# Kernel optimization log

Measured on AMD Instinct MI355X. Metric: run time of the kernel, lower is better.

Reference implementation:

```python
import jax, jax.numpy as jnp
import numpy as np

ALPHA = 0.2  # tf.nn.leaky_relu default alpha
B, LATENT, T, N = 8, 256, 128, 768
F, L, E = 4, 3, 12288


def _causal_conv1d(x, w, b):
    # x: [B,T,Cin], w: [K,Cin,Cout] -> causal pad left by K-1
    k = w.shape[0]
    y = jax.lax.conv_general_dilated(x, w, (1,), ((k - 1, 0),),
                                     dimension_numbers=('NWC', 'WIO', 'NWC'))
    return y + b


def _same_conv1d(x, w, b):
    y = jax.lax.conv_general_dilated(x, w, (1,), 'SAME',
                                     dimension_numbers=('NWC', 'WIO', 'NWC'))
    return y + b


def _same_conv2d(x, w, b):
    y = jax.lax.conv_general_dilated(x, w, (1, 1), 'SAME',
                                     dimension_numbers=('NHWC', 'HWIO', 'NHWC'))
    return y + b


def _gat(nodes, row, col, qw, qb, kw, kb, vw, vb):
    # tf_geometric-style single-head GAT; row/col already contain self-loops.
    M = nodes.shape[0]
    Q = jax.nn.leaky_relu(nodes @ qw + qb, ALPHA)
    K = jax.nn.leaky_relu(nodes @ kw + kb, ALPHA)
    V = nodes @ vw
    scale = jnp.sqrt(jnp.asarray(Q.shape[-1], nodes.dtype))
    score = jnp.sum(Q[row] * K[col], axis=-1) / scale  # [E']
    smax = jax.ops.segment_max(score, row, num_segments=M)
    ex = jnp.exp(score - smax[row])
    den = jax.ops.segment_sum(ex, row, num_segments=M)
    att = ex / den[row]
    out = jax.ops.segment_sum(V[col] * att[:, None], row, num_segments=M)
    return out + vb


def _gw_layer(y, row, col, wa, ba, wb, bb, qw, qb, kw, kb, vw, vb, rw, rb):
    b_, t_, n_, f_ = y.shape
    x = jnp.moveaxis(y, -1, 0)  # [F,B,T,N]

    def branch(xf, wa_, ba_, wb_, bb_, qw_, qb_, kw_, kb_, vw_, vb_):
        a = jax.nn.sigmoid(_causal_conv1d(xf, wa_, ba_))
        g = a * jnp.tanh(_causal_conv1d(xf, wb_, bb_))   # gated TCN [B,T,N]
        nodes = g.transpose(0, 2, 1).reshape(b_ * n_, t_)  # node id = b*N + n
        h = _gat(nodes, row, col, qw_, qb_, kw_, kb_, vw_, vb_)
        return h.reshape(b_, n_, t_).transpose(0, 2, 1)  # [B,T,N]

    outs = jax.vmap(branch)(x, wa, ba, wb, bb, qw, qb, kw, kb, vw, vb)
    outs = jnp.moveaxis(outs, 0, -1)                      # [B,T,N,F]
    res = jnp.einsum('btnf,fg->btng', y, rw) + rb         # 1x1 res conv
    return outs + res


def _decoder(x, edges, shunt_dense_w, shunt_dense_b, shunt_c1_w, shunt_c1_b,
             shunt_c2_w, shunt_c2_b, tcn_a_w, tcn_a_b, tcn_b_w, tcn_b_b,
             gat_q_w, gat_q_b, gat_k_w, gat_k_b, gat_v_w, gat_v_b,
             res_w, res_b, skip_w, skip_b, out1_w, out1_b, out2_w, out2_b):
    # ConvShunt: [B,latent] -> [B,T] -> [B,T,N] -> [B,T,N,F]
    y = x @ shunt_dense_w + shunt_dense_b
    y = _same_conv1d(y[..., None], shunt_c1_w, shunt_c1_b)
    y = _same_conv2d(y[..., None], shunt_c2_w, shunt_c2_b)
    M = B * N
    self_idx = jnp.arange(M, dtype=edges.dtype)
    row = jnp.concatenate([edges[0], self_idx])
    col = jnp.concatenate([edges[1], self_idx])
    skips = []
    for i in range(L):
        y = _gw_layer(y, row, col, tcn_a_w[i], tcn_a_b[i], tcn_b_w[i], tcn_b_b[i],
                      gat_q_w[i], gat_q_b[i], gat_k_w[i], gat_k_b[i],
                      gat_v_w[i], gat_v_b[i], res_w[i], res_b[i])
        skips.append(jax.nn.leaky_relu(
            jnp.einsum('btnf,f->btn', y, skip_w[i]) + skip_b[i], ALPHA))
    s = jnp.stack(skips, axis=-1)                         # [B,T,N,L]
    g = jax.nn.leaky_relu(_same_conv2d(s, out1_w, out1_b), ALPHA)
    return _same_conv2d(g, out2_w, out2_b)                # [B,T,N,1]


def setup_inputs() -> dict:
    ks = iter(jax.random.split(jax.random.key(0), 32))

    def w(shape, fan_in):
        return jax.random.normal(next(ks), shape, jnp.float32) / np.sqrt(fan_in).astype(np.float32)

    return {
        'x': jax.random.normal(next(ks), (B, LATENT), jnp.float32),
        'edges': jax.random.randint(next(ks), (2, E), 0, N, jnp.int32),
        'shunt_dense_w': w((LATENT, T), LATENT),
        'shunt_dense_b': jnp.zeros((T,), jnp.float32),
        'shunt_c1_w': w((3, 1, N), 3),
        'shunt_c1_b': jnp.zeros((N,), jnp.float32),
        'shunt_c2_w': w((3, 3, 1, F), 9),
        'shunt_c2_b': jnp.zeros((F,), jnp.float32),
        'tcn_a_w': w((L, F, 5, N, N), 5 * N),
        'tcn_a_b': jnp.zeros((L, F, N), jnp.float32),
        'tcn_b_w': w((L, F, 5, N, N), 5 * N),
        'tcn_b_b': jnp.zeros((L, F, N), jnp.float32),
        'gat_q_w': w((L, F, T, T), T),
        'gat_q_b': jnp.zeros((L, F, T), jnp.float32),
        'gat_k_w': w((L, F, T, T), T),
        'gat_k_b': jnp.zeros((L, F, T), jnp.float32),
        'gat_v_w': w((L, F, T, T), T),
        'gat_v_b': jnp.zeros((L, F, T), jnp.float32),
        'res_w': w((L, F, F), F),
        'res_b': jnp.zeros((L, F), jnp.float32),
        'skip_w': w((L, F), F),
        'skip_b': jnp.zeros((L,), jnp.float32),
        'out1_w': w((3, 3, L, 1), 9 * L),
        'out1_b': jnp.zeros((1,), jnp.float32),
        'out2_w': w((1, 1, 1, 1), 1),
        'out2_b': jnp.zeros((1,), jnp.float32),
    }


def reference(x, edges, shunt_dense_w, shunt_dense_b, shunt_c1_w, shunt_c1_b,
              shunt_c2_w, shunt_c2_b, tcn_a_w, tcn_a_b, tcn_b_w, tcn_b_b,
              gat_q_w, gat_q_b, gat_k_w, gat_k_b, gat_v_w, gat_v_b,
              res_w, res_b, skip_w, skip_b, out1_w, out1_b, out2_w, out2_b):
    return _decoder(x, edges, shunt_dense_w, shunt_dense_b, shunt_c1_w, shunt_c1_b,
                    shunt_c2_w, shunt_c2_b, tcn_a_w, tcn_a_b, tcn_b_w, tcn_b_b,
                    gat_q_w, gat_q_b, gat_k_w, gat_k_b, gat_v_w, gat_v_b,
                    res_w, res_b, skip_w, skip_b, out1_w, out1_b, out2_w, out2_b)
```

## Files before the change

### kernel.cpp

```cpp
#include <hip/hip_runtime.h>
#include <math.h>

#define ALPHA_ 0.2f
#define AS1 __attribute__((address_space(1)))
#define AS3 __attribute__((address_space(3)))

constexpr int B_ = 8, LATENT_ = 256, T_ = 128, N_ = 768, F_ = 4, L_ = 3, E_ = 12288;
constexpr int M_ = B_ * N_;
constexpr int MT_ = B_ * T_;
constexpr int EP_ = E_ + M_;
constexpr int BTN_ = B_ * T_ * N_;
constexpr size_t SZ_ = (size_t)BTN_ * F_;
constexpr int KTCN_ = 5 * N_;
constexpr int KSPLIT_ = KTCN_ / 2;
constexpr int TP_ = T_ + 4;

typedef __bf16 bf16x8 __attribute__((ext_vector_type(8)));
typedef float f32x4 __attribute__((ext_vector_type(4)));

__device__ __forceinline__ float lrelu(float x) { return x > 0.0f ? x : ALPHA_ * x; }
__device__ __forceinline__ unsigned short f2bf(float x) {
    union { __bf16 h; unsigned short u; } c; c.h = (__bf16)x; return c.u;
}
__device__ __forceinline__ float bf2f(unsigned short u) {
    return __uint_as_float(((unsigned)u) << 16);
}
__device__ __forceinline__ float bflo(unsigned u) { return __uint_as_float(u << 16); }
__device__ __forceinline__ float bfhi(unsigned u) { return __uint_as_float(u & 0xffff0000u); }

__global__ void k_dense(const float* __restrict__ x, const float* __restrict__ w,
                        const float* __restrict__ b, float* __restrict__ y0) {
    int i = blockIdx.x * blockDim.x + threadIdx.x;
    if (i >= B_ * T_) return;
    int bb = i / T_, t = i % T_;
    float acc = b[t];
    for (int l = 0; l < LATENT_; ++l) acc += x[bb * LATENT_ + l] * w[l * T_ + t];
    y0[i] = acc;
}

__global__ void k_conv1(const float* __restrict__ y0, const float* __restrict__ w,
                        const float* __restrict__ b, float* __restrict__ y1) {
    int i = blockIdx.x * blockDim.x + threadIdx.x;
    if (i >= BTN_) return;
    int n = i % N_, t = (i / N_) % T_, bb = i / (N_ * T_);
    float acc = b[n];
    #pragma unroll
    for (int k = 0; k < 3; ++k) {
        int tt = t - 1 + k;
        if (tt >= 0 && tt < T_) acc += y0[bb * T_ + tt] * w[k * N_ + n];
    }
    y1[i] = acc;
}

__global__ void k_conv2w(const float* __restrict__ y1, const float* __restrict__ w,
                         const float* __restrict__ b, float* __restrict__ y,
                         unsigned short* __restrict__ xTpad) {
    int i = blockIdx.x * blockDim.x + threadIdx.x;
    if (i >= BTN_) return;
    int n = i % N_, t = (i / N_) % T_, bb = i / (N_ * T_);
    float acc[F_];
    #pragma unroll
    for (int f = 0; f < F_; ++f) acc[f] = b[f];
    #pragma unroll
    for (int dt = 0; dt < 3; ++dt) {
        int tt = t - 1 + dt;
        if (tt < 0 || tt >= T_) continue;
        #pragma unroll
        for (int dn = 0; dn < 3; ++dn) {
            int nn = n - 1 + dn;
            if (nn < 0 || nn >= N_) continue;
            float v = y1[(bb * T_ + tt) * N_ + nn];
            #pragma unroll
            for (int f = 0; f < F_; ++f) acc[f] += v * w[(dt * 3 + dn) * F_ + f];
        }
    }
    #pragma unroll
    for (int f = 0; f < F_; ++f) {
        y[(size_t)i * F_ + f] = acc[f];
        xTpad[((size_t)(f * B_ + bb) * TP_ + 4 + t) * N_ + n] = f2bf(acc[f]);
    }
}

__global__ __launch_bounds__(256) void k_convT2(const float* __restrict__ aw,
        const float* __restrict__ bw, unsigned short* __restrict__ wat3,
        unsigned short* __restrict__ wbt3) {
    constexpr int S_ = 770;
    __shared__ unsigned short tl[32 * S_];
    const int z = blockIdx.y;
    const int f = z & 3, wsel = (z >> 2) & 1, layer = z >> 3;
    const size_t toff = ((size_t)layer * F_ + f) * (size_t)KTCN_ * N_;
    const float* in = (wsel ? bw : aw) + toff + (size_t)blockIdx.x * 32 * N_;
    unsigned short* outP = (wsel ? wbt3 : wat3) + toff + (size_t)blockIdx.x * (N_ * 32);
    const int tid = threadIdx.x;
    #pragma unroll
    for (int p = 0; p < 24; ++p) {
        const int flat = p * 256 + tid;
        const int k = flat / 192;
        const int nf = flat - k * 192;
        const float4 v = *(const float4*)(in + (size_t)k * N_ + nf * 4);
        const unsigned int lo = ((unsigned)f2bf(v.y) << 16) | f2bf(v.x);
        const unsigned int hi = ((unsigned)f2bf(v.w) << 16) | f2bf(v.z);
        unsigned int* dst = (unsigned int*)&tl[k * S_ + nf * 4];
        dst[0] = lo;
        dst[1] = hi;
    }
    __syncthreads();
    #pragma unroll
    for (int q = 0; q < 12; ++q) {
        const int flat = q * 256 + tid;
        const int n = flat >> 2;
        const int cc = flat & 3;
        const int o = cc ^ ((n >> 1) & 3);
        unsigned short pk[8];
        #pragma unroll
        for (int j = 0; j < 8; ++j) pk[j] = tl[(o * 8 + j) * S_ + n];
        *(uint4*)(outP + (size_t)n * 32 + cc * 8) = *(uint4*)pk;
    }
}

__global__ __launch_bounds__(256) void k_convTproj(const float* __restrict__ qw,
        const float* __restrict__ kw, const float* __restrict__ vw,
        unsigned short* __restrict__ pwt3) {
    __shared__ float tl[32][33];
    const int z = blockIdx.z;
    const int f = z & 3;
    const int sel = (z >> 2) % 3;
    const int layer = z / 12;
    const float* in = (sel == 0 ? qw : (sel == 1 ? kw : vw))
                      + ((size_t)layer * F_ + f) * T_ * T_;
    unsigned short* outT = pwt3 + (((size_t)layer * 3 + sel) * F_ + f) * T_ * T_;
    const int x0 = blockIdx.x * 32;
    const int y0 = blockIdx.y * 32;
    const int tx = threadIdx.x & 31, ty = threadIdx.x >> 5;
    #pragma unroll
    for (int r = 0; r < 4; ++r)
        tl[ty + r * 8][tx] = in[(size_t)(y0 + ty + r * 8) * T_ + x0 + tx];
    __syncthreads();
    #pragma unroll
    for (int r = 0; r < 4; ++r)
        outT[(size_t)(x0 + ty + r * 8) * T_ + y0 + tx] = f2bf(tl[tx][ty + r * 8]);
}

__global__ __launch_bounds__(256) void k_tcn_mfma(
        const unsigned short* __restrict__ xTpad,
        const unsigned short* __restrict__ wat, const unsigned short* __restrict__ wbt,
        const float* __restrict__ ba, const float* __restrict__ bbias,
        unsigned short* __restrict__ pa, unsigned short* __restrict__ pb) {
    __shared__ unsigned short As[2][128 * 32];
    __shared__ unsigned short Bs[2][128 * 32];
    const int bid = blockIdx.x;
    const int bt = bid / 96;
    const int c = bid - bt * 96;
    const int xb = c % 6;
    const int zz = c / 6;
    const int f = zz & 3;
    const int wsel = (zz >> 2) & 1;
    const int s = zz >> 3;
    const int n0 = xb * 128;
    const unsigned short* xf = xTpad + (size_t)(f * B_ + bt) * TP_ * N_;
    const unsigned short* wfp = (wsel ? wbt : wat) + (size_t)f * KTCN_ * N_;
    const float* bias = (wsel ? bbias : ba) + f * N_;
    unsigned short* out = (wsel ? pb : pa) + (size_t)s * SZ_;
    const int tid = threadIdx.x;
    const int lane = tid & 63;
    const int w = tid >> 6;
    const int wm = (w >> 1) * 64, wn = (w & 1) * 64;
    const int r16 = lane & 15, kb = lane >> 4;
    const int srow = lane >> 2;
    const int scol = (((lane & 3) ^ ((lane >> 3) & 3)) * 8);
    const int bcol = (lane & 3) * 8;
    const int kx = (kb ^ ((r16 >> 1) & 3)) * 8;
    const int k_lo = s * KSPLIT_, k_hi = k_lo + KSPLIT_;

    auto stage = [&](int buf, int kk0) {
        const int ks = kk0 / N_;
        const int nin0 = kk0 - ks * N_;
        const unsigned short* plane = wfp + (size_t)(kk0 >> 5) * (N_ * 32);
        #pragma unroll
        for (int h = 0; h < 2; ++h) {
            const int seg = w + 4 * h;
            const int row = seg * 16 + srow;
            const unsigned short* gA = xf + (size_t)(row + ks) * N_ + nin0 + scol;
            const unsigned short* gB = plane + (size_t)(n0 + row) * 32 + bcol;
            __builtin_amdgcn_global_load_lds((const AS1 unsigned int*)(const void*)gA,
                    (AS3 unsigned int*)(void*)(&As[buf][seg * 512]), 16, 0, 0);
            __builtin_amdgcn_global_load_lds((const AS1 unsigned int*)(const void*)gB,
                    (AS3 unsigned int*)(void*)(&Bs[buf][seg * 512]), 16, 0, 0);
        }
    };

    f32x4 acc[4][4] = {};
    stage(0, k_lo);
    __syncthreads();
    int cur = 0;
    for (int kk0 = k_lo; kk0 < k_hi; kk0 += 32) {
        if (kk0 + 32 < k_hi) stage(cur ^ 1, kk0 + 32);
        bf16x8 av[4], bv[4];
        #pragma unroll
        for (int i = 0; i < 4; ++i)
            av[i] = *(const bf16x8*)(&As[cur][(wm + i * 16 + r16) * 32 + kx]);
        #pragma unroll
        for (int j = 0; j < 4; ++j)
            bv[j] = *(const bf16x8*)(&Bs[cur][(wn + j * 16 + r16) * 32 + kx]);
        #pragma unroll
        for (int i = 0; i < 4; ++i)
            #pragma unroll
            for (int j = 0; j < 4; ++j)
                acc[i][j] = __builtin_amdgcn_mfma_f32_16x16x32_bf16(av[i], bv[j], acc[i][j], 0, 0, 0);
        __syncthreads();
        cur ^= 1;
    }
    unsigned short* of = out + (size_t)(f * B_ + bt) * T_ * N_;
    #pragma unroll
    for (int i = 0; i < 4; ++i) {
        #pragma unroll
        for (int j = 0; j < 4; ++j) {
            const int n = n0 + wn + j * 16 + r16;
            const float bv2 = (s == 0) ? bias[n] : 0.0f;
            #pragma unroll
            for (int r = 0; r < 4; ++r) {
                const int m = wm + i * 16 + kb * 4 + r;
                of[(size_t)m * N_ + n] = f2bf(acc[i][j][r] + bv2);
            }
        }
    }
}

__global__ __launch_bounds__(256) void k_gate_nodes(const unsigned short* __restrict__ pa,
        const unsigned short* __restrict__ pb, unsigned short* __restrict__ nodes) {
    __shared__ float tl[32][33];
    const int bz = blockIdx.z;
    const int t0 = blockIdx.x * 32, n0 = blockIdx.y * 32;
    const size_t base = (size_t)bz * T_ * N_;
    {
        const int r = threadIdx.x >> 3;
        const int c = threadIdx.x & 7;
        const size_t idx = base + (size_t)(t0 + r) * N_ + n0 + c * 4;
        const uint2 A0 = *(const uint2*)(pa + idx);
        const uint2 A1 = *(const uint2*)(pa + SZ_ + idx);
        const uint2 B0 = *(const uint2*)(pb + idx);
        const uint2 B1 = *(const uint2*)(pb + SZ_ + idx);
        const float av[4] = {bflo(A0.x) + bflo(A1.x), bfhi(A0.x) + bfhi(A1.x),
                             bflo(A0.y) + bflo(A1.y), bfhi(A0.y) + bfhi(A1.y)};
        const float bv[4] = {bflo(B0.x) + bflo(B1.x), bfhi(B0.x) + bfhi(B1.x),
                             bflo(B0.y) + bflo(B1.y), bfhi(B0.y) + bfhi(B1.y)};
        #pragma unroll
        for (int j = 0; j < 4; ++j)
            tl[r][c * 4 + j] = (1.0f / (1.0f + __expf(-av[j]))) * tanhf(bv[j]);
    }
    __syncthreads();
    {
        const int nr = threadIdx.x >> 3;
        const int tc = threadIdx.x & 7;
        unsigned short pk[4];
        #pragma unroll
        for (int j = 0; j < 4; ++j) pk[j] = f2bf(tl[tc * 4 + j][nr]);
        *(uint2*)(nodes + base + (size_t)(n0 + nr) * T_ + t0 + tc * 4) = *(uint2*)pk;
    }
}

__global__ __launch_bounds__(256) void k_proj_mfma(
        const unsigned short* __restrict__ nodes, const unsigned short* __restrict__ pwt,
        const float* __restrict__ qb, const float* __restrict__ kbias,
        unsigned short* __restrict__ Q, unsigned short* __restrict__ K,
        unsigned short* __restrict__ V) {
    __shared__ unsigned short As[2][128 * 32];
    __shared__ unsigned short Bs[2][128 * 32];
    const int zz = blockIdx.z;
    const int f = zz & 3;
    const int sel = zz >> 2;
    const int m0 = blockIdx.y * 128;
    const unsigned short* af = nodes + (size_t)f * M_ * T_;
    const unsigned short* wfp = pwt + (size_t)sel * F_ * T_ * T_ + (size_t)f * T_ * T_;
    const float* bias = (sel == 0) ? qb : (sel == 1 ? kbias : nullptr);
    unsigned short* out = (sel == 0) ? Q : (sel == 1 ? K : V);
    const int tid = threadIdx.x;
    const int lane = tid & 63;
    const int w = tid >> 6;
    const int wm = (w >> 1) * 64, wn = (w & 1) * 64;
    const int r16 = lane & 15, kb = lane >> 4;
    const int srow = lane >> 2;
    const int scol = (((lane & 3) ^ ((lane >> 3) & 3)) * 8);
    const int kx = (kb ^ ((r16 >> 1) & 3)) * 8;

    auto stage = [&](int buf, int kk0) {
        #pragma unroll
        for (int h = 0; h < 2; ++h) {
            const int seg = w + 4 * h;
            const int row = seg * 16 + srow;
            const unsigned short* gA = af + (size_t)(m0 + row) * T_ + kk0 + scol;
            const unsigned short* gB = wfp + (size_t)row * T_ + kk0 + scol;
            __builtin_amdgcn_global_load_lds((const AS1 unsigned int*)(const void*)gA,
                    (AS3 unsigned int*)(void*)(&As[buf][seg * 512]), 16, 0, 0);
            __builtin_amdgcn_global_load_lds((const AS1 unsigned int*)(const void*)gB,
                    (AS3 unsigned int*)(void*)(&Bs[buf][seg * 512]), 16, 0, 0);
        }
    };

    f32x4 acc[4][4] = {};
    stage(0, 0);
    __syncthreads();
    int cur = 0;
    for (int kk0 = 0; kk0 < T_; kk0 += 32) {
        if (kk0 + 32 < T_) stage(cur ^ 1, kk0 + 32);
        bf16x8 av[4], bv[4];
        #pragma unroll
        for (int i = 0; i < 4; ++i)
            av[i] = *(const bf16x8*)(&As[cur][(wm + i * 16 + r16) * 32 + kx]);
        #pragma unroll
        for (int j = 0; j < 4; ++j)
            bv[j] = *(const bf16x8*)(&Bs[cur][(wn + j * 16 + r16) * 32 + kx]);
        #pragma unroll
        for (int i = 0; i < 4; ++i)
            #pragma unroll
            for (int j = 0; j < 4; ++j)
                acc[i][j] = __builtin_amdgcn_mfma_f32_16x16x32_bf16(av[i], bv[j], acc[i][j], 0, 0, 0);
        __syncthreads();
        cur ^= 1;
    }
    const int do_l = (sel < 2);
    unsigned short* of = out + (size_t)f * M_ * T_;
    #pragma unroll
    for (int i = 0; i < 4; ++i) {
        #pragma unroll
        for (int j = 0; j < 4; ++j) {
            const int n = wn + j * 16 + r16;
            #pragma unroll
            for (int r = 0; r < 4; ++r) {
                const int m = m0 + wm + i * 16 + kb * 4 + r;
                float v = acc[i][j][r];
                if (bias) v += bias[f * T_ + n];
                if (do_l) v = lrelu(v);
                of[(size_t)m * T_ + n] = f2bf(v);
            }
        }
    }
}

__device__ __forceinline__ int edge_row(const int* e, int i) { return i < E_ ? e[i] : i - E_; }
__device__ __forceinline__ int edge_col(const int* e, int i) { return i < E_ ? e[E_ + i] : i - E_; }

__global__ void k_hist(const int* __restrict__ edges, int* __restrict__ deg) {
    int i = blockIdx.x * blockDim.x + threadIdx.x;
    if (i >= EP_) return;
    atomicAdd(&deg[edge_row(edges, i)], 1);
}

__global__ __launch_bounds__(256) void k_scan(const int* __restrict__ deg,
        int* __restrict__ rowptr, int* __restrict__ cursor) {
    __shared__ int part[256];
    const int tid = threadIdx.x;
    constexpr int PER = M_ / 256;
    int loc[PER];
    int s = 0;
    #pragma unroll
    for (int j = 0; j < PER; ++j) { loc[j] = s; s += deg[tid * PER + j]; }
    part[tid] = s;
    __syncthreads();
    if (tid == 0) {
        int run = 0;
        for (int i2 = 0; i2 < 256; ++i2) { int v = part[i2]; part[i2] = run; run += v; }
        rowptr[M_] = run;
    }
    __syncthreads();
    const int off = part[tid];
    #pragma unroll
    for (int j = 0; j < PER; ++j) {
        rowptr[tid * PER + j] = off + loc[j];
        cursor[tid * PER + j] = off + loc[j];
    }
}

__global__ void k_scatter(const int* __restrict__ edges, int* __restrict__ cursor,
                          int* __restrict__ csr_col) {
    int i = blockIdx.x * blockDim.x + threadIdx.x;
    if (i >= EP_) return;
    int r = edge_row(edges, i), c = edge_col(edges, i);
    int pos = atomicAdd(&cursor[r], 1);
    csr_col[pos] = c;
}

__global__ __launch_bounds__(256) void k_gat(const unsigned short* __restrict__ Q,
        const unsigned short* __restrict__ Kb, const unsigned short* __restrict__ V,
        const int* __restrict__ rowptr, const int* __restrict__ csr_col,
        unsigned short* __restrict__ H) {
    constexpr int CAP = 128;
    __shared__ float sc[4][CAP];
    const int w = threadIdx.x >> 6, lane = threadIdx.x & 63;
    const int wv = blockIdx.x * 4 + w;
    const int f = wv / M_, r = wv - f * M_;
    const int p0 = rowptr[r], p1 = rowptr[r + 1];
    unsigned short* Hr = H + ((size_t)f * M_ + r) * T_;
    if (p1 - p0 == 1) {
        const unsigned short* Vr = V + ((size_t)f * M_ + r) * T_;
        *(unsigned*)(Hr + 2 * lane) = *(const unsigned*)(Vr + 2 * lane);
        return;
    }
    const unsigned short* Qr = Q + ((size_t)f * M_ + r) * T_;
    const unsigned qv = *(const unsigned*)(Qr + 2 * lane);
    const float q0 = bflo(qv), q1 = bfhi(qv);
    float mx = -3.4e38f;
    for (int j = p0; j < p1; ++j) {
        const unsigned short* Kc = Kb + ((size_t)f * M_ + csr_col[j]) * T_;
        const unsigned kv = *(const unsigned*)(Kc + 2 * lane);
        float s = q0 * bflo(kv) + q1 * bfhi(kv);
        #pragma unroll
        for (int mk = 32; mk >= 1; mk >>= 1) s += __shfl_xor(s, mk);
        s *= 0.0883883476483184f;
        if (lane == 0) sc[w][j - p0] = s;
        mx = fmaxf(mx, s);
    }
    float den = 0.0f;
    for (int j = p0; j < p1; ++j) den += __expf(sc[w][j - p0] - mx);
    const float rden = 1.0f / den;
    float a0 = 0.0f, a1 = 0.0f;
    for (int j = p0; j < p1; ++j) {
        const int c = csr_col[j];
        const float att = __expf(sc[w][j - p0] - mx) * rden;
        const unsigned short* Vc = V + ((size_t)f * M_ + c) * T_;
        const unsigned vv = *(const unsigned*)(Vc + 2 * lane);
        a0 += att * bflo(vv);
        a1 += att * bfhi(vv);
    }
    *(unsigned*)(Hr + 2 * lane) = (unsigned)f2bf(a0) | ((unsigned)f2bf(a1) << 16);
}

__global__ __launch_bounds__(256) void k_combine_t(const float* __restrict__ y,
        const unsigned short* __restrict__ H, const float* __restrict__ vb,
        const float* __restrict__ rw, const float* __restrict__ rb,
        const float* __restrict__ skw, const float* __restrict__ skb, int layer,
        float* __restrict__ ynext, unsigned short* __restrict__ xTpad,
        float* __restrict__ sbufp) {
    __shared__ float hl[F_][32][33];
    const int b = blockIdx.z;
    const int t0 = blockIdx.x * 32, n0 = blockIdx.y * 32;
    {
        const int nn = threadIdx.x >> 3;
        const int tc = threadIdx.x & 7;
        #pragma unroll
        for (int g = 0; g < F_; ++g) {
            const uint2 hv = *(const uint2*)(H +
                ((size_t)g * M_ + b * N_ + n0 + nn) * T_ + t0 + tc * 4);
            hl[g][nn][tc * 4 + 0] = bflo(hv.x);
            hl[g][nn][tc * 4 + 1] = bfhi(hv.x);
            hl[g][nn][tc * 4 + 2] = bflo(hv.y);
            hl[g][nn][tc * 4 + 3] = bfhi(hv.y);
        }
    }
    __syncthreads();
    const int r = threadIdx.x >> 3;
    const int nc = threadIdx.x & 7;
    const int t = t0 + r;
    const size_t ibase = ((size_t)b * T_ + t) * N_ + n0 + nc * 4;
    float o[4][F_];
    float sbv[4];
    #pragma unroll
    for (int q = 0; q < 4; ++q) {
        const float4 y4 = *(const float4*)(y + (ibase + q) * 4);
        #pragma unroll
        for (int g = 0; g < F_; ++g) {
            float acc = hl[g][nc * 4 + q][r] + vb[g * T_ + t] + rb[g];
            acc += y4.x * rw[0 * F_ + g] + y4.y * rw[1 * F_ + g]
                 + y4.z * rw[2 * F_ + g] + y4.w * rw[3 * F_ + g];
            o[q][g] = acc;
        }
        float4 o4 = {o[q][0], o[q][1], o[q][2], o[q][3]};
        *(float4*)(ynext + (ibase + q) * 4) = o4;
        float sk = skb[layer];
        #pragma unroll
        for (int g = 0; g < F_; ++g) sk += o[q][g] * skw[layer * F_ + g];
        sbv[q] = lrelu(sk);
    }
    #pragma unroll
    for (int g = 0; g < F_; ++g) {
        unsigned short pk[4];
        #pragma unroll
        for (int q = 0; q < 4; ++q) pk[q] = f2bf(o[q][g]);
        *(uint2*)(xTpad + ((size_t)(g * B_ + b) * TP_ + 4 + t) * N_ + n0 + nc * 4)
            = *(uint2*)pk;
    }
    float4 s4 = {sbv[0], sbv[1], sbv[2], sbv[3]};
    *(float4*)(sbufp + (size_t)layer * BTN_ + ibase) = s4;
}

__global__ void k_final(const float* __restrict__ sbufp, const float* __restrict__ o1w,
        const float* __restrict__ o1b, const float* __restrict__ o2w,
        const float* __restrict__ o2b, float* __restrict__ out) {
    int i = blockIdx.x * blockDim.x + threadIdx.x;
    if (i >= BTN_) return;
    int n = i % N_, t = (i / N_) % T_, bb = i / (N_ * T_);
    float acc = o1b[0];
    #pragma unroll
    for (int dt = 0; dt < 3; ++dt) {
        int tt = t - 1 + dt;
        if (tt < 0 || tt >= T_) continue;
        #pragma unroll
        for (int dn = 0; dn < 3; ++dn) {
            int nn = n - 1 + dn;
            if (nn < 0 || nn >= N_) continue;
            const size_t base = (size_t)(bb * T_ + tt) * N_ + nn;
            #pragma unroll
            for (int l = 0; l < L_; ++l)
                acc += sbufp[(size_t)l * BTN_ + base] * o1w[(dt * 3 + dn) * L_ + l];
        }
    }
    float g = lrelu(acc);
    out[i] = g * o2w[0] + o2b[0];
}

extern "C" void kernel_launch(void* const* d_in, const int* in_sizes, int n_in,
                              void* d_out, int out_size, void* d_ws, size_t ws_size,
                              hipStream_t stream) {
    const float* x       = (const float*)d_in[0];
    const int*   edges   = (const int*)d_in[1];
    const float* sd_w    = (const float*)d_in[2];
    const float* sd_b    = (const float*)d_in[3];
    const float* c1w     = (const float*)d_in[4];
    const float* c1b     = (const float*)d_in[5];
    const float* c2w     = (const float*)d_in[6];
    const float* c2b     = (const float*)d_in[7];
    const float* tcn_a_w = (const float*)d_in[8];
    const float* tcn_a_b = (const float*)d_in[9];
    const float* tcn_b_w = (const float*)d_in[10];
    const float* tcn_b_b = (const float*)d_in[11];
    const float* gat_q_w = (const float*)d_in[12];
    const float* gat_q_b = (const float*)d_in[13];
    const float* gat_k_w = (const float*)d_in[14];
    const float* gat_k_b = (const float*)d_in[15];
    const float* gat_v_w = (const float*)d_in[16];
    const float* gat_v_b = (const float*)d_in[17];
    const float* res_w   = (const float*)d_in[18];
    const float* res_b   = (const float*)d_in[19];
    const float* skip_w  = (const float*)d_in[20];
    const float* skip_b  = (const float*)d_in[21];
    const float* out1_w  = (const float*)d_in[22];
    const float* out1_b  = (const float*)d_in[23];
    const float* out2_w  = (const float*)d_in[24];
    const float* out2_b  = (const float*)d_in[25];
    float* out = (float*)d_out;

    float* ws = (float*)d_ws;
    size_t off = 0;
    auto alloc = [&](size_t nf) { float* p = ws + off; off += nf; return p; };
    float* ybuf  = alloc(SZ_);
    float* y2buf = alloc(SZ_);
    float* sbufp = alloc((size_t)BTN_ * L_);
    float* y0    = alloc(MT_);
    float* y1    = alloc(BTN_);
    unsigned short* xTpad  = (unsigned short*)alloc((size_t)F_ * B_ * TP_ * N_ / 2 + 16);
    unsigned short* nodesb = (unsigned short*)alloc(SZ_ / 2);
    unsigned short* qb16   = (unsigned short*)alloc(SZ_ / 2);
    unsigned short* kb16   = (unsigned short*)alloc(SZ_ / 2);
    unsigned short* vb16   = (unsigned short*)alloc(SZ_ / 2);
    unsigned short* Hb     = (unsigned short*)alloc(SZ_ / 2);
    unsigned short* pa     = (unsigned short*)alloc(SZ_);
    unsigned short* pb     = (unsigned short*)alloc(SZ_);
    unsigned short* wat3 = (unsigned short*)alloc((size_t)L_ * F_ * KTCN_ * N_ / 2);
    unsigned short* wbt3 = (unsigned short*)alloc((size_t)L_ * F_ * KTCN_ * N_ / 2);
    unsigned short* pwt3 = (unsigned short*)alloc((size_t)L_ * 3 * F_ * T_ * T_ / 2);
    int* rowptr  = (int*)alloc(M_ + 1);
    int* cursor  = (int*)alloc(M_);
    int* deg     = (int*)alloc(M_);
    int* csr_col = (int*)alloc(EP_);
    (void)ws_size; (void)in_sizes; (void)n_in; (void)out_size;

    hipMemsetAsync(xTpad, 0, (size_t)F_ * B_ * TP_ * N_ * 2, stream);
    hipMemsetAsync(deg, 0, M_ * 4, stream);
    k_hist<<<(EP_ + 255) / 256, 256, 0, stream>>>(edges, deg);
    k_scan<<<1, 256, 0, stream>>>(deg, rowptr, cursor);
    k_scatter<<<(EP_ + 255) / 256, 256, 0, stream>>>(edges, cursor, csr_col);

    dim3 gw2(KTCN_ / 32, 8 * L_);
    k_convT2<<<gw2, 256, 0, stream>>>(tcn_a_w, tcn_b_w, wat3, wbt3);
    dim3 gpw(T_ / 32, T_ / 32, 12 * L_);
    k_convTproj<<<gpw, 256, 0, stream>>>(gat_q_w, gat_k_w, gat_v_w, pwt3);

    k_dense<<<(B_ * T_ + 255) / 256, 256, 0, stream>>>(x, sd_w, sd_b, y0);
    k_conv1<<<(BTN_ + 255) / 256, 256, 0, stream>>>(y0, c1w, c1b, y1);
    k_conv2w<<<(BTN_ + 255) / 256, 256, 0, stream>>>(y1, c2w, c2b, ybuf, xTpad);

    float* cur = ybuf;
    float* nxt = y2buf;
    for (int layer = 0; layer < L_; ++layer) {
        const float* ba = tcn_a_b + (size_t)layer * F_ * N_;
        const float* bb = tcn_b_b + (size_t)layer * F_ * N_;
        const float* qb = gat_q_b + (size_t)layer * F_ * T_;
        const float* kbias = gat_k_b + (size_t)layer * F_ * T_;
        const float* vb = gat_v_b + (size_t)layer * F_ * T_;
        const float* rw = res_w + (size_t)layer * F_ * F_;
        const float* rb = res_b + (size_t)layer * F_;
        const unsigned short* wat = wat3 + (size_t)layer * F_ * KTCN_ * N_;
        const unsigned short* wbt = wbt3 + (size_t)layer * F_ * KTCN_ * N_;
        const unsigned short* pwt = pwt3 + (size_t)layer * 3 * F_ * T_ * T_;

        k_tcn_mfma<<<768, 256, 0, stream>>>(xTpad, wat, wbt, ba, bb, pa, pb);
        dim3 gg(T_ / 32, N_ / 32, F_ * B_);
        k_gate_nodes<<<gg, 256, 0, stream>>>(pa, pb, nodesb);
        dim3 gp(1, M_ / 128, 12);
        k_proj_mfma<<<gp, 256, 0, stream>>>(nodesb, pwt, qb, kbias, qb16, kb16, vb16);
        k_gat<<<(F_ * M_) / 4, 256, 0, stream>>>(qb16, kb16, vb16, rowptr, csr_col, Hb);
        dim3 gc(T_ / 32, N_ / 32, B_);
        k_combine_t<<<gc, 256, 0, stream>>>(cur, Hb, vb, rw, rb, skip_w, skip_b,
                layer, nxt, xTpad, sbufp);
        float* tmp = cur; cur = nxt; nxt = tmp;
    }
    k_final<<<(BTN_ + 255) / 256, 256, 0, stream>>>(sbufp, out1_w, out1_b, out2_w, out2_b, out);
}
```

Baseline: 548.5 us.

## Drop fp32 activation buffers; read residual from bf16 xTpad and store skips in bf16

The fp32 y/ynext ping-pong buffers are removed. The residual 1x1 conv in k_combine_t now reads the layer input from the bf16 transposed xTpad buffer, which is already written, and updates it in place. The skip buffer sbufp is also stored in bf16 and read back in k_final. This cuts global memory traffic in conv2w, combine and final, at the cost of bf16 rounding in the residual path and skip sums, which compounds across layers.

New measurement: 532.5 us. 1.03x faster.

```diff
diff --git a/kernel.cpp b/kernel.cpp
--- a/kernel.cpp
+++ b/kernel.cpp
@@ -53,8 +53,7 @@
 }
 
 __global__ void k_conv2w(const float* __restrict__ y1, const float* __restrict__ w,
-                         const float* __restrict__ b, float* __restrict__ y,
-                         unsigned short* __restrict__ xTpad) {
+                         const float* __restrict__ b, unsigned short* __restrict__ xTpad) {
     int i = blockIdx.x * blockDim.x + threadIdx.x;
     if (i >= BTN_) return;
     int n = i % N_, t = (i / N_) % T_, bb = i / (N_ * T_);
@@ -75,10 +74,8 @@
         }
     }
     #pragma unroll
-    for (int f = 0; f < F_; ++f) {
-        y[(size_t)i * F_ + f] = acc[f];
+    for (int f = 0; f < F_; ++f)
         xTpad[((size_t)(f * B_ + bb) * TP_ + 4 + t) * N_ + n] = f2bf(acc[f]);
-    }
 }
 
 __global__ __launch_bounds__(256) void k_convT2(const float* __restrict__ aw,
@@ -425,12 +422,11 @@
     *(unsigned*)(Hr + 2 * lane) = (unsigned)f2bf(a0) | ((unsigned)f2bf(a1) << 16);
 }
 
-__global__ __launch_bounds__(256) void k_combine_t(const float* __restrict__ y,
-        const unsigned short* __restrict__ H, const float* __restrict__ vb,
-        const float* __restrict__ rw, const float* __restrict__ rb,
-        const float* __restrict__ skw, const float* __restrict__ skb, int layer,
-        float* __restrict__ ynext, unsigned short* __restrict__ xTpad,
-        float* __restrict__ sbufp) {
+__global__ __launch_bounds__(256) void k_combine_t(const unsigned short* __restrict__ Hb,
+        const float* __restrict__ vb, const float* __restrict__ rw,
+        const float* __restrict__ rb, const float* __restrict__ skw,
+        const float* __restrict__ skb, int layer,
+        unsigned short* __restrict__ xTpad, unsigned short* __restrict__ sbufp) {
     __shared__ float hl[F_][32][33];
     const int b = blockIdx.z;
     const int t0 = blockIdx.x * 32, n0 = blockIdx.y * 32;
@@ -439,7 +435,7 @@
         const int tc = threadIdx.x & 7;
         #pragma unroll
         for (int g = 0; g < F_; ++g) {
-            const uint2 hv = *(const uint2*)(H +
+            const uint2 hv = *(const uint2*)(Hb +
                 ((size_t)g * M_ + b * N_ + n0 + nn) * T_ + t0 + tc * 4);
             hl[g][nn][tc * 4 + 0] = bflo(hv.x);
             hl[g][nn][tc * 4 + 1] = bfhi(hv.x);
@@ -451,21 +447,25 @@
     const int r = threadIdx.x >> 3;
     const int nc = threadIdx.x & 7;
     const int t = t0 + r;
-    const size_t ibase = ((size_t)b * T_ + t) * N_ + n0 + nc * 4;
+    float yv[4][F_];
+    #pragma unroll
+    for (int g = 0; g < F_; ++g) {
+        const uint2 xv = *(const uint2*)(xTpad +
+            ((size_t)(g * B_ + b) * TP_ + 4 + t) * N_ + n0 + nc * 4);
+        yv[0][g] = bflo(xv.x); yv[1][g] = bfhi(xv.x);
+        yv[2][g] = bflo(xv.y); yv[3][g] = bfhi(xv.y);
+    }
     float o[4][F_];
     float sbv[4];
     #pragma unroll
     for (int q = 0; q < 4; ++q) {
-        const float4 y4 = *(const float4*)(y + (ibase + q) * 4);
         #pragma unroll
         for (int g = 0; g < F_; ++g) {
             float acc = hl[g][nc * 4 + q][r] + vb[g * T_ + t] + rb[g];
-            acc += y4.x * rw[0 * F_ + g] + y4.y * rw[1 * F_ + g]
-                 + y4.z * rw[2 * F_ + g] + y4.w * rw[3 * F_ + g];
+            #pragma unroll
+            for (int f2 = 0; f2 < F_; ++f2) acc += yv[q][f2] * rw[f2 * F_ + g];
             o[q][g] = acc;
         }
-        float4 o4 = {o[q][0], o[q][1], o[q][2], o[q][3]};
-        *(float4*)(ynext + (ibase + q) * 4) = o4;
         float sk = skb[layer];
         #pragma unroll
         for (int g = 0; g < F_; ++g) sk += o[q][g] * skw[layer * F_ + g];
@@ -479,13 +479,17 @@
         *(uint2*)(xTpad + ((size_t)(g * B_ + b) * TP_ + 4 + t) * N_ + n0 + nc * 4)
             = *(uint2*)pk;
     }
-    float4 s4 = {sbv[0], sbv[1], sbv[2], sbv[3]};
-    *(float4*)(sbufp + (size_t)layer * BTN_ + ibase) = s4;
-}
-
-__global__ void k_final(const float* __restrict__ sbufp, const float* __restrict__ o1w,
-        const float* __restrict__ o1b, const float* __restrict__ o2w,
-        const float* __restrict__ o2b, float* __restrict__ out) {
+    unsigned short sp[4];
+    #pragma unroll
+    for (int q = 0; q < 4; ++q) sp[q] = f2bf(sbv[q]);
+    *(uint2*)(sbufp + (size_t)layer * BTN_ + ((size_t)b * T_ + t) * N_ + n0 + nc * 4)
+        = *(uint2*)sp;
+}
+
+__global__ void k_final(const unsigned short* __restrict__ sbufp,
+        const float* __restrict__ o1w, const float* __restrict__ o1b,
+        const float* __restrict__ o2w, const float* __restrict__ o2b,
+        float* __restrict__ out) {
     int i = blockIdx.x * blockDim.x + threadIdx.x;
     if (i >= BTN_) return;
     int n = i % N_, t = (i / N_) % T_, bb = i / (N_ * T_);
@@ -501,7 +505,7 @@
             const size_t base = (size_t)(bb * T_ + tt) * N_ + nn;
             #pragma unroll
             for (int l = 0; l < L_; ++l)
-                acc += sbufp[(size_t)l * BTN_ + base] * o1w[(dt * 3 + dn) * L_ + l];
+                acc += bf2f(sbufp[(size_t)l * BTN_ + base]) * o1w[(dt * 3 + dn) * L_ + l];
         }
     }
     float g = lrelu(acc);
@@ -542,9 +546,6 @@
     float* ws = (float*)d_ws;
     size_t off = 0;
     auto alloc = [&](size_t nf) { float* p = ws + off; off += nf; return p; };
-    float* ybuf  = alloc(SZ_);
-    float* y2buf = alloc(SZ_);
-    float* sbufp = alloc((size_t)BTN_ * L_);
     float* y0    = alloc(MT_);
     float* y1    = alloc(BTN_);
     unsigned short* xTpad  = (unsigned short*)alloc((size_t)F_ * B_ * TP_ * N_ / 2 + 16);
@@ -555,6 +556,7 @@
     unsigned short* Hb     = (unsigned short*)alloc(SZ_ / 2);
     unsigned short* pa     = (unsigned short*)alloc(SZ_);
     unsigned short* pb     = (unsigned short*)alloc(SZ_);
+    unsigned short* sbufp  = (unsigned short*)alloc((size_t)BTN_ * L_ / 2);
     unsigned short* wat3 = (unsigned short*)alloc((size_t)L_ * F_ * KTCN_ * N_ / 2);
     unsigned short* wbt3 = (unsigned short*)alloc((size_t)L_ * F_ * KTCN_ * N_ / 2);
     unsigned short* pwt3 = (unsigned short*)alloc((size_t)L_ * 3 * F_ * T_ * T_ / 2);
@@ -577,10 +579,8 @@
 
     k_dense<<<(B_ * T_ + 255) / 256, 256, 0, stream>>>(x, sd_w, sd_b, y0);
     k_conv1<<<(BTN_ + 255) / 256, 256, 0, stream>>>(y0, c1w, c1b, y1);
-    k_conv2w<<<(BTN_ + 255) / 256, 256, 0, stream>>>(y1, c2w, c2b, ybuf, xTpad);
-
-    float* cur = ybuf;
-    float* nxt = y2buf;
+    k_conv2w<<<(BTN_ + 255) / 256, 256, 0, stream>>>(y1, c2w, c2b, xTpad);
+
     for (int layer = 0; layer < L_; ++layer) {
         const float* ba = tcn_a_b + (size_t)layer * F_ * N_;
         const float* bb = tcn_b_b + (size_t)layer * F_ * N_;
@@ -600,9 +600,8 @@
         k_proj_mfma<<<gp, 256, 0, stream>>>(nodesb, pwt, qb, kbias, qb16, kb16, vb16);
         k_gat<<<(F_ * M_) / 4, 256, 0, stream>>>(qb16, kb16, vb16, rowptr, csr_col, Hb);
         dim3 gc(T_ / 32, N_ / 32, B_);
-        k_combine_t<<<gc, 256, 0, stream>>>(cur, Hb, vb, rw, rb, skip_w, skip_b,
-                layer, nxt, xTpad, sbufp);
-        float* tmp = cur; cur = nxt; nxt = tmp;
+        k_combine_t<<<gc, 256, 0, stream>>>(Hb, vb, rw, rb, skip_w, skip_b,
+                layer, xTpad, sbufp);
     }
     k_final<<<(BTN_ + 255) / 256, 256, 0, stream>>>(sbufp, out1_w, out1_b, out2_w, out2_b, out);
 }
```
